# Kernel optimization log

Hardware: AMD Instinct MI355X
Metric: run time of the kernel (lower is better)

Reference implementation:

```python
import jax, jax.numpy as jnp
import numpy as np

PI = jnp.pi
NB_FRAMES = 2


def _axis_angle_to_R(r):
    # r: [..., 3] axis-angle -> rotation matrix [..., 3, 3] (Rodrigues)
    eps = 1e-8
    theta = jnp.sqrt(jnp.sum(r * r, axis=-1, keepdims=True))  # [...,1]
    k = r / jnp.maximum(theta, eps)
    kx, ky, kz = k[..., 0], k[..., 1], k[..., 2]
    zero = jnp.zeros_like(kx)
    K = jnp.stack([
        jnp.stack([zero, -kz, ky], axis=-1),
        jnp.stack([kz, zero, -kx], axis=-1),
        jnp.stack([-ky, kx, zero], axis=-1),
    ], axis=-2)  # [...,3,3]
    I = jnp.eye(3, dtype=r.dtype)
    s = jnp.sin(theta)[..., None]
    c = jnp.cos(theta)[..., None]
    return I + s * K + (1.0 - c) * (K @ K)


def _equirec_dirs(h, w, dtype):
    # unit viewing directions of an equirectangular grid, [h, w, 3]
    lon = ((jnp.arange(w, dtype=dtype) + 0.5) / w * 2.0 - 1.0) * PI
    lat = -((jnp.arange(h, dtype=dtype) + 0.5) / h * 2.0 - 1.0) * (0.5 * PI)
    LON, LAT = jnp.meshgrid(lon, lat)  # [h, w]
    dx = jnp.cos(LAT) * jnp.sin(LON)
    dy = jnp.sin(LAT)
    dz = jnp.cos(LAT) * jnp.cos(LON)
    return jnp.stack([dx, dy, dz], axis=-1)


def _grid_sample(img, grid):
    # img: [B,C,H,W]; grid: [B,Hg,Wg,2] in [-1,1] (x,y); bilinear,
    # align_corners=True, zero padding (matches F.grid_sample defaults)
    B, C, H, W = img.shape
    x = (grid[..., 0] + 1.0) * 0.5 * (W - 1)
    y = (grid[..., 1] + 1.0) * 0.5 * (H - 1)
    x0 = jnp.floor(x)
    y0 = jnp.floor(y)
    x1 = x0 + 1.0
    y1 = y0 + 1.0
    img_flat = img.reshape(B, C, H * W)

    def gather(xi, yi):
        valid = (xi >= 0) & (xi <= W - 1) & (yi >= 0) & (yi <= H - 1)
        xc = jnp.clip(xi, 0, W - 1).astype(jnp.int32)
        yc = jnp.clip(yi, 0, H - 1).astype(jnp.int32)
        idx = (yc * W + xc).reshape(B, 1, -1)
        v = jnp.take_along_axis(img_flat, idx, axis=2).reshape(B, C, *xi.shape[1:])
        return v * valid[:, None].astype(img.dtype)

    wa = ((x1 - x) * (y1 - y))[:, None]
    wb = ((x1 - x) * (y - y0))[:, None]
    wc = ((x - x0) * (y1 - y))[:, None]
    wd = ((x - x0) * (y - y0))[:, None]
    return (gather(x0, y0) * wa + gather(x0, y1) * wb +
            gather(x1, y0) * wc + gather(x1, y1) * wd)


def _area_down(x, s):
    # F.interpolate(mode='area') with integer factor == average pooling
    if s == 1:
        return x
    B, C, H, W = x.shape
    return x.reshape(B, C, H // s, s, W // s, s).mean(axis=(3, 5))


def _photometric_loss(ref_rgb, depths, masks, tgts, pose):
    R = _axis_angle_to_R(pose[..., 3:])      # [B, nb, 3, 3]
    t = pose[..., :3]                         # [B, nb, 3]
    loss = jnp.zeros((), dtype=ref_rgb.dtype)
    for i, (d, m) in enumerate(zip(depths, masks)):
        s = 2 ** i
        h, w = d.shape[2], d.shape[3]
        rr = _area_down(ref_rgb, s)                       # [B,3,h,w]
        tg = [_area_down(tr, s) for tr in tgts]
        dirs = _equirec_dirs(h, w, ref_rgb.dtype)         # [h,w,3]
        xyz = d[:, 0, :, :, None] * dirs[None]            # [B,h,w,3]
        # pose transform: pts = R @ xyz + t  -> [B,h,w,nb,3]
        pts = jnp.einsum('bnij,bhwj->bhwni', R, xyz) + t[:, None, None]
        norm = jnp.sqrt(jnp.sum(pts * pts, axis=-1))
        lon = jnp.arctan2(pts[..., 0], pts[..., 2])
        lat = jnp.arcsin(jnp.clip(pts[..., 1] / jnp.maximum(norm, 1e-8), -1.0, 1.0))
        X = lon / PI                  # [B,h,w,nb]
        Y = lat / (0.5 * PI)
        for j in range(NB_FRAMES):
            coord = jnp.stack([X[..., j], Y[..., j]], axis=-1)  # [B,h,w,2]
            wf = _grid_sample(tg[j], coord)                     # [B,3,h,w]
            loss = loss + jnp.mean(m[:, j:j + 1] * jnp.abs(rr - wf))
    return loss


def setup_inputs() -> dict:
    key = jax.random.key(0)
    ks = jax.random.split(key, 16)
    B, H, W = 8, 512, 1024
    inp = {'ref_rgb': jax.random.uniform(ks[0], (B, 3, H, W), jnp.float32)}
    for i in range(4):
        h, w = H // (2 ** i), W // (2 ** i)
        inp[f'ref_depth{i}'] = jax.random.uniform(ks[1 + i], (B, 1, h, w), jnp.float32)
        inp[f'exp_mask{i}'] = jax.random.uniform(ks[5 + i], (B, NB_FRAMES, h, w), jnp.float32)
    inp['tgt_rgb0'] = jax.random.uniform(ks[9], (B, 3, H, W), jnp.float32)
    inp['tgt_rgb1'] = jax.random.uniform(ks[10], (B, 3, H, W), jnp.float32)
    inp['pose'] = jax.random.normal(ks[11], (B, NB_FRAMES, 6), jnp.float32)
    return inp


def reference(ref_rgb, ref_depth0, ref_depth1, ref_depth2, ref_depth3,
              exp_mask0, exp_mask1, exp_mask2, exp_mask3,
              tgt_rgb0, tgt_rgb1, pose):
    depths = [ref_depth0, ref_depth1, ref_depth2, ref_depth3]
    masks = [exp_mask0, exp_mask1, exp_mask2, exp_mask3]
    tgts = [tgt_rgb0, tgt_rgb1]
    return _photometric_loss(ref_rgb, depths, masks, tgts, pose)
```

## Files before the change

kernel.cpp:

```cpp
#include <hip/hip_runtime.h>
#include <hip/hip_fp16.h>
#include <math.h>

#define PI_F 3.14159265358979323846f

__device__ inline float fast_atan2f(float y, float x) {
    float ax = fabsf(x), ay = fabsf(y);
    float mx = fmaxf(ax, ay);
    float mn = fminf(ax, ay);
    float a = __fdividef(mn, fmaxf(mx, 1e-30f));
    float s = a * a;
    float r = fmaf(s, fmaf(s, fmaf(s, fmaf(s, fmaf(s, -0.01172120f, 0.05265332f),
                   -0.11643287f), 0.19354346f), -0.33262347f), 0.99997726f);
    r = r * a;
    if (ay > ax) r = 1.57079632679f - r;
    if (x < 0.0f) r = PI_F - r;
    return copysignf(r, y);
}

__device__ inline float fast_atanp(float y, float x) {
    float ay = fabsf(y);
    float mx = fmaxf(x, ay);
    float mn = fminf(x, ay);
    float a = __fdividef(mn, fmaxf(mx, 1e-30f));
    float s = a * a;
    float r = fmaf(s, fmaf(s, fmaf(s, fmaf(s, fmaf(s, -0.01172120f, 0.05265332f),
                   -0.11643287f), 0.19354346f), -0.33262347f), 0.99997726f);
    r = r * a;
    if (ay > x) r = 1.57079632679f - r;
    return copysignf(r, y);
}

__device__ inline void make_Rt_to(const float* __restrict__ pose, int bn, float* __restrict__ o) {
    const float* p = pose + bn * 6;
    float tx = p[0], ty = p[1], tz = p[2];
    float rx = p[3], ry = p[4], rz = p[5];
    float theta = sqrtf(rx * rx + ry * ry + rz * rz);
    float inv = __fdividef(1.0f, fmaxf(theta, 1e-8f));
    float kx = rx * inv, ky = ry * inv, kz = rz * inv;
    float s, c;
    __sincosf(theta, &s, &c);
    float oc = 1.0f - c;
    o[0] = 1.0f - oc * (ky * ky + kz * kz);
    o[1] = -s * kz + oc * kx * ky;
    o[2] =  s * ky + oc * kx * kz;
    o[3] =  s * kz + oc * kx * ky;
    o[4] = 1.0f - oc * (kx * kx + kz * kz);
    o[5] = -s * kx + oc * ky * kz;
    o[6] = -s * ky + oc * kx * kz;
    o[7] =  s * kx + oc * ky * kz;
    o[8] = 1.0f - oc * (kx * kx + ky * ky);
    o[9] = tx; o[10] = ty; o[11] = tz;
}

__device__ inline unsigned pack_px1(float r, float g, float b) {
    unsigned ri = __float2uint_rn(__saturatef(r) * 2047.0f);
    unsigned gi = __float2uint_rn(__saturatef(g) * 2047.0f);
    unsigned bi = __float2uint_rn(__saturatef(b) * 1023.0f);
    return ri | (gi << 11) | (bi << 22);
}
__device__ inline float3 unpack_fields(unsigned u) {
    float r = (float)(u & 2047u);
    float g = (float)((u >> 11) & 2047u);
    float b = (float)(u >> 22);
    return make_float3(r, g, b);
}

typedef struct __attribute__((packed, aligned(4))) { unsigned x, y; } upair;

__global__ __launch_bounds__(256) void prep_kernel(
    const float* __restrict__ ref, const float* __restrict__ tgt0, const float* __restrict__ tgt1,
    unsigned* __restrict__ packF,
    unsigned* __restrict__ pL1t, unsigned* __restrict__ pL2t, unsigned* __restrict__ pL3t,
    unsigned* __restrict__ pL1r, unsigned* __restrict__ pL2r, unsigned* __restrict__ pL3r,
    float* __restrict__ out)
{
    int bid = blockIdx.x;
    int t = threadIdx.x;
    if (bid == 0 && t == 0) out[0] = 0.0f;
    int i = bid % 3;
    int rem = bid / 3;
    int b = rem & 7;
    int band = rem >> 3;
    const float* img = (i == 0) ? ref : (i == 1) ? tgt0 : tgt1;
    int x4 = t << 2;
    int y0 = band << 3;
    int q = (i - 1) * 8 + b;

    float l1v[4][2][3];
#pragma unroll
    for (int p = 0; p < 4; ++p) {
        float4 a[3], bb[3];
#pragma unroll
        for (int c = 0; c < 3; ++c) {
            const float* pl = img + ((size_t)(b * 3 + c) << 19);
            a[c]  = *(const float4*)(pl + ((y0 + 2 * p) << 10) + x4);
            bb[c] = *(const float4*)(pl + ((y0 + 2 * p + 1) << 10) + x4);
        }
        if (i > 0) {
            unsigned* o = packF + ((size_t)q << 19) + ((y0 + 2 * p) << 10) + x4;
            uint4 v0;
            v0.x = pack_px1(a[0].x, a[1].x, a[2].x);
            v0.y = pack_px1(a[0].y, a[1].y, a[2].y);
            v0.z = pack_px1(a[0].z, a[1].z, a[2].z);
            v0.w = pack_px1(a[0].w, a[1].w, a[2].w);
            *(uint4*)o = v0;
            unsigned* o2 = o + (1 << 10);
            uint4 v1;
            v1.x = pack_px1(bb[0].x, bb[1].x, bb[2].x);
            v1.y = pack_px1(bb[0].y, bb[1].y, bb[2].y);
            v1.z = pack_px1(bb[0].z, bb[1].z, bb[2].z);
            v1.w = pack_px1(bb[0].w, bb[1].w, bb[2].w);
            *(uint4*)o2 = v1;
        }
#pragma unroll
        for (int c = 0; c < 3; ++c) {
            l1v[p][0][c] = (a[c].x + a[c].y + bb[c].x + bb[c].y) * 0.25f;
            l1v[p][1][c] = (a[c].z + a[c].w + bb[c].z + bb[c].w) * 0.25f;
        }
        uint2 d;
        d.x = pack_px1(l1v[p][0][0], l1v[p][0][1], l1v[p][0][2]);
        d.y = pack_px1(l1v[p][1][0], l1v[p][1][1], l1v[p][1][2]);
        unsigned* d1 = ((i == 0) ? pL1r + ((size_t)b << 17) : pL1t + ((size_t)q << 17))
                    + (((band << 2) + p) << 9) + (t << 1);
        *(uint2*)d1 = d;
    }
    float l2v[2][3];
#pragma unroll
    for (int pr = 0; pr < 2; ++pr) {
#pragma unroll
        for (int c = 0; c < 3; ++c)
            l2v[pr][c] = (l1v[2 * pr][0][c] + l1v[2 * pr][1][c] +
                          l1v[2 * pr + 1][0][c] + l1v[2 * pr + 1][1][c]) * 0.25f;
        unsigned* d2 = ((i == 0) ? pL2r + ((size_t)b << 15) : pL2t + ((size_t)q << 15))
                    + (((band << 1) + pr) << 8) + t;
        *d2 = pack_px1(l2v[pr][0], l2v[pr][1], l2v[pr][2]);
    }
    float l3[3];
#pragma unroll
    for (int c = 0; c < 3; ++c) {
        float s = l2v[0][c] + l2v[1][c];
        l3[c] = (s + __shfl_xor(s, 1)) * 0.25f;
    }
    if ((t & 1) == 0) {
        unsigned* d3 = ((i == 0) ? pL3r + ((size_t)b << 13) : pL3t + ((size_t)q << 13))
                    + (band << 7) + (t >> 1);
        *d3 = pack_px1(l3[0], l3[1], l3[2]);
    }
}

template <int SH>
__device__ inline float photo_scale4(int bidl, int tid,
                                     const float* __restrict__ rrF,
                                     const unsigned* __restrict__ rrP,
                                     const float* __restrict__ depth,
                                     const float* __restrict__ mask,
                                     const unsigned* __restrict__ tg,
                                     const float* __restrict__ pose,
                                     float* __restrict__ ldsRt) {
    constexpr int h = 512 >> SH;
    constexpr int w = 1024 >> SH;
    constexpr int LOG2W = 10 - SH;
    constexpr int LP = 19 - 2 * SH;
    constexpr float inv_count = 1.0f / (8.0f * 3.0f * h * w);
    constexpr float GXS = (float)((w - 1) / (2.0 * 3.14159265358979323846));
    constexpr float GXB = (float)((w - 1) * 0.5);
    constexpr float GYS = (float)((h - 1) / 3.14159265358979323846);
    constexpr float GYB = (float)((h - 1) * 0.5);
    constexpr float CDs[4] = {0.9999811752826011f, 0.9999247018391445f,
                              0.9996988186962042f, 0.9987954562051724f};
    constexpr float SDs[4] = {0.006135884649154475f, 0.012271538285719925f,
                              0.024541228522912288f, 0.049067674327418015f};
    constexpr float CD = CDs[SH], SD = SDs[SH];

    int lidx = ((bidl << 8) + tid) << 2;
    int b = lidx >> LP;
    if (tid < 2) make_Rt_to(pose, b * 2 + tid, ldsRt + tid * 12);
    __syncthreads();

    int x0 = lidx & (w - 1);
    int y = (lidx >> LOG2W) & (h - 1);
    int pix = (y << LOG2W) + x0;

    float lat = -(((float)y + 0.5f) * (2.0f / (float)h) - 1.0f) * (0.5f * PI_F);
    float slat = __sinf(lat), clat = __cosf(lat);

    float4 dep4 = *(const float4*)(depth + ((size_t)b << LP) + pix);
    float dp[4] = {dep4.x, dep4.y, dep4.z, dep4.w};
    float rcv[4][3];
    if constexpr (SH == 0) {
#pragma unroll
        for (int c = 0; c < 3; ++c) {
            float F = (c == 2) ? 1023.0f : 2047.0f;
            float4 rv = *(const float4*)(rrF + ((size_t)(b * 3 + c) << LP) + pix);
            rcv[0][c] = rv.x * F; rcv[1][c] = rv.y * F;
            rcv[2][c] = rv.z * F; rcv[3][c] = rv.w * F;
        }
    } else {
        const unsigned* rp = rrP + ((size_t)b << LP) + pix;
        uint4 u = *(const uint4*)rp;
        float3 f0 = unpack_fields(u.x), f1 = unpack_fields(u.y);
        float3 f2 = unpack_fields(u.z), f3 = unpack_fields(u.w);
        rcv[0][0] = f0.x; rcv[0][1] = f0.y; rcv[0][2] = f0.z;
        rcv[1][0] = f1.x; rcv[1][1] = f1.y; rcv[1][2] = f1.z;
        rcv[2][0] = f2.x; rcv[2][1] = f2.y; rcv[2][2] = f2.z;
        rcv[3][0] = f3.x; rcv[3][1] = f3.y; rcv[3][2] = f3.z;
    }
    float m4[2][4];
#pragma unroll
    for (int n = 0; n < 2; ++n) {
        float4 mv = *(const float4*)(mask + ((size_t)(b * 2 + n) << LP) + pix);
        m4[n][0] = mv.x; m4[n][1] = mv.y; m4[n][2] = mv.z; m4[n][3] = mv.w;
    }

    const unsigned* pl0 = tg + ((size_t)b << LP);
    const unsigned* pl1 = tg + ((size_t)(8 + b) << LP);

    float fxv[8], fyv[8];
    int off2[8][2];
    float lon0 = (((float)x0 + 0.5f) * (2.0f / (float)w) - 1.0f) * PI_F;
    float sl, cl;
    __sincosf(lon0, &sl, &cl);
#pragma unroll
    for (int i = 0; i < 4; ++i) {
        if (i > 0) {
            float s2 = fmaf(sl, CD, cl * SD);
            float c2 = fmaf(cl, CD, -sl * SD);
            sl = s2; cl = c2;
        }
        float X = dp[i] * (clat * sl);
        float Y = dp[i] * slat;
        float Z = dp[i] * (clat * cl);
#pragma unroll
        for (int n = 0; n < 2; ++n) {
            const float* R = ldsRt + n * 12;
            float px = fmaf(R[0], X, fmaf(R[1], Y, fmaf(R[2], Z, R[9])));
            float py = fmaf(R[3], X, fmaf(R[4], Y, fmaf(R[5], Z, R[10])));
            float pz = fmaf(R[6], X, fmaf(R[7], Y, fmaf(R[8], Z, R[11])));
            float rxz2 = fmaf(px, px, pz * pz);
            float rxz = rxz2 * __frsqrt_rn(fmaxf(rxz2, 1e-30f));
            float lon2 = fast_atan2f(px, pz);
            float lat2 = fast_atanp(py, rxz);
            float gx = fmaf(lon2, GXS, GXB);
            float gy = fmaf(lat2, GYS, GYB);
            float x0f = floorf(gx), y0f = floorf(gy);
            int xi0 = max((int)x0f, 0);
            int yi0 = max((int)y0f, 0);
            int yi1 = min(yi0 + 1, h - 1);
            int g = i * 2 + n;
            fxv[g] = gx - x0f;
            fyv[g] = gy - y0f;
            off2[g][0] = (yi0 << LOG2W) + xi0;
            off2[g][1] = (yi1 << LOG2W) + xi0;
        }
    }
    upair tp[8][2];
#pragma unroll
    for (int g = 0; g < 8; ++g) {
        const unsigned* P = (g & 1) ? pl1 : pl0;
        tp[g][0] = *(const upair*)(P + off2[g][0]);
        tp[g][1] = *(const upair*)(P + off2[g][1]);
    }
    float acc = 0.0f;
#pragma unroll
    for (int g = 0; g < 8; ++g) {
        int i = g >> 1, n = g & 1;
        float fx = fxv[g], fy = fyv[g];
        float ofx = 1.0f - fx, ofy = 1.0f - fy;
        float w00 = ofx * ofy;
        float w01 = ofx * fy;
        float w10 = fx * ofy;
        float w11 = fx * fy;
        float3 ta = unpack_fields(tp[g][0].x);
        float3 tc = unpack_fields(tp[g][0].y);
        float3 tb = unpack_fields(tp[g][1].x);
        float3 td = unpack_fields(tp[g][1].y);
        float d0 = rcv[i][0] - (fmaf(w00, ta.x, fmaf(w01, tb.x, fmaf(w10, tc.x, w11 * td.x))));
        float d1 = rcv[i][1] - (fmaf(w00, ta.y, fmaf(w01, tb.y, fmaf(w10, tc.y, w11 * td.y))));
        float d2 = rcv[i][2] - (fmaf(w00, ta.z, fmaf(w01, tb.z, fmaf(w10, tc.z, w11 * td.z))));
        float t = fabsf(d0) * (1.0f / 2047.0f);
        t = fmaf(fabsf(d1), (1.0f / 2047.0f), t);
        t = fmaf(fabsf(d2), (1.0f / 1023.0f), t);
        acc = fmaf(m4[n][i], t, acc);
    }
    return acc * inv_count;
}

__global__ __launch_bounds__(256) void photo_all_packed4q(
    const float* __restrict__ rrF,
    const unsigned* __restrict__ rr1, const unsigned* __restrict__ rr2, const unsigned* __restrict__ rr3,
    const float* __restrict__ dep0, const float* __restrict__ msk0,
    const float* __restrict__ dep1, const float* __restrict__ msk1,
    const float* __restrict__ dep2, const float* __restrict__ msk2,
    const float* __restrict__ dep3, const float* __restrict__ msk3,
    const unsigned* __restrict__ packF,
    const unsigned* __restrict__ pL1t, const unsigned* __restrict__ pL2t, const unsigned* __restrict__ pL3t,
    const float* __restrict__ pose, float* __restrict__ out) {
    __shared__ float ldsRt[24];
    __shared__ float wsum[4];
    int bid = blockIdx.x, tid = threadIdx.x;
    float acc;
    if (bid < 4096) {
        int s = ((bid & 7) << 9) | (bid >> 3);
        acc = photo_scale4<0>(s, tid, rrF, nullptr, dep0, msk0, packF, pose, ldsRt);
    } else if (bid < 5120) {
        int t0 = bid - 4096;
        int s = ((t0 & 7) << 7) | (t0 >> 3);
        acc = photo_scale4<1>(s, tid, nullptr, rr1, dep1, msk1, pL1t, pose, ldsRt);
    } else if (bid < 5376) {
        int t0 = bid - 5120;
        int s = ((t0 & 7) << 5) | (t0 >> 3);
        acc = photo_scale4<2>(s, tid, nullptr, rr2, dep2, msk2, pL2t, pose, ldsRt);
    } else {
        int t0 = bid - 5376;
        int s = ((t0 & 7) << 3) | (t0 >> 3);
        acc = photo_scale4<3>(s, tid, nullptr, rr3, dep3, msk3, pL3t, pose, ldsRt);
    }

    for (int off = 32; off > 0; off >>= 1) acc += __shfl_down(acc, off);
    if ((tid & 63) == 0) wsum[tid >> 6] = acc;
    __syncthreads();
    if (tid == 0) atomicAdd(out, wsum[0] + wsum[1] + wsum[2] + wsum[3]);
}

template <int LWD>
__global__ __launch_bounds__(256) void down3_kernel(const float* __restrict__ sA,
                                                    const float* __restrict__ sB,
                                                    const float* __restrict__ sC,
                                                    float* __restrict__ dA,
                                                    float* __restrict__ dB,
                                                    float* __restrict__ dC) {
    const float* src = (blockIdx.y == 0) ? sA : (blockIdx.y == 1) ? sB : sC;
    float* dst = (blockIdx.y == 0) ? dA : (blockIdx.y == 1) ? dB : dC;
    int idx = blockIdx.x * 256 + threadIdx.x;
    constexpr int HB = LWD - 1;
    int xp = idx & ((1 << HB) - 1);
    int y = (idx >> HB) & ((1 << HB) - 1);
    int c = idx >> (2 * HB);
    const float* sp = src + ((size_t)c << (2 * LWD + 1)) + ((size_t)(2 * y) << (LWD + 1)) + 4 * xp;
    float4 r0 = *(const float4*)sp;
    float4 r1 = *(const float4*)(sp + (1 << (LWD + 1)));
    float2 d;
    d.x = 0.25f * (r0.x + r0.y + r1.x + r1.y);
    d.y = 0.25f * (r0.z + r0.w + r1.z + r1.w);
    *(float2*)(dst + ((size_t)c << (2 * LWD - 1)) + ((size_t)y << LWD) + 2 * xp) = d;
}

template <int SH>
__device__ inline float photo_scale(int bidl, int tid,
                                    const float* __restrict__ rr,
                                    const float* __restrict__ depth,
                                    const float* __restrict__ mask,
                                    const float* __restrict__ tg0,
                                    const float* __restrict__ tg1,
                                    const float* __restrict__ pose,
                                    float* __restrict__ ldsRt) {
    constexpr int h = 512 >> SH;
    constexpr int w = 1024 >> SH;
    constexpr int LOG2W = 10 - SH;
    constexpr int LP = 19 - 2 * SH;
    constexpr float inv_count = 1.0f / (8.0f * 3.0f * h * w);
    int lidx = (bidl << 8) + tid;
    int b = lidx >> LP;
    if (tid < 2) make_Rt_to(pose, b * 2 + tid, ldsRt + tid * 12);
    __syncthreads();
    int x = lidx & (w - 1);
    int y = (lidx >> LOG2W) & (h - 1);
    int pix = (y << LOG2W) + x;
    float lon = (((float)x + 0.5f) * (2.0f / (float)w) - 1.0f) * PI_F;
    float lat = -(((float)y + 0.5f) * (2.0f / (float)h) - 1.0f) * (0.5f * PI_F);
    float sl = __sinf(lon), cl = __cosf(lon);
    float slat = __sinf(lat), clat = __cosf(lat);
    float dep = depth[((size_t)b << LP) + pix];
    float X = dep * clat * sl, Y = dep * slat, Z = dep * clat * cl;
    float rc[3];
#pragma unroll
    for (int c = 0; c < 3; ++c)
        rc[c] = rr[((size_t)(b * 3 + c) << LP) + pix];
    float acc = 0.0f;
#pragma unroll
    for (int n = 0; n < 2; ++n) {
        const float* R = ldsRt + n * 12;
        float px = R[0] * X + R[1] * Y + R[2] * Z + R[9];
        float py = R[3] * X + R[4] * Y + R[5] * Z + R[10];
        float pz = R[6] * X + R[7] * Y + R[8] * Z + R[11];
        float rxz = sqrtf(px * px + pz * pz);
        float lon2 = fast_atan2f(px, pz);
        float lat2 = fast_atan2f(py, rxz);
        float gx = (lon2 * (1.0f / PI_F) + 1.0f) * 0.5f * (float)(w - 1);
        float gy = (lat2 * (2.0f / PI_F) + 1.0f) * 0.5f * (float)(h - 1);
        float x0f = floorf(gx), y0f = floorf(gy);
        float fx = gx - x0f, fy = gy - y0f;
        float wa = (1.0f - fx) * (1.0f - fy);
        float wb = (1.0f - fx) * fy;
        float wc = fx * (1.0f - fy);
        float wd = fx * fy;
        bool vx0 = (x0f >= 0.0f) && (x0f <= (float)(w - 1));
        bool vx1 = (x0f >= -1.0f) && (x0f <= (float)(w - 2));
        bool vy0 = (y0f >= 0.0f) && (y0f <= (float)(h - 1));
        bool vy1 = (y0f >= -1.0f) && (y0f <= (float)(h - 2));
        int xi0 = (int)fminf(fmaxf(x0f, 0.0f), (float)(w - 1));
        int xi1 = (int)fminf(fmaxf(x0f + 1.0f, 0.0f), (float)(w - 1));
        int yi0 = (int)fminf(fmaxf(y0f, 0.0f), (float)(h - 1));
        int yi1 = (int)fminf(fmaxf(y0f + 1.0f, 0.0f), (float)(h - 1));
        float waf = (vx0 && vy0) ? wa : 0.0f;
        float wbf = (vx0 && vy1) ? wb : 0.0f;
        float wcf = (vx1 && vy0) ? wc : 0.0f;
        float wdf = (vx1 && vy1) ? wd : 0.0f;
        int ia = (yi0 << LOG2W) + xi0;
        int ib2 = (yi1 << LOG2W) + xi0;
        int ic = (yi0 << LOG2W) + xi1;
        int id = (yi1 << LOG2W) + xi1;
        const float* tg = (n == 0) ? tg0 : tg1;
        float m = mask[((size_t)(b * 2 + n) << LP) + pix];
#pragma unroll
        for (int c = 0; c < 3; ++c) {
            const float* plane = tg + ((size_t)(b * 3 + c) << LP);
            float v = waf * plane[ia] + wbf * plane[ib2] + wcf * plane[ic] + wdf * plane[id];
            acc += m * fabsf(rc[c] - v);
        }
    }
    return acc * inv_count;
}

__global__ __launch_bounds__(256) void photo_all_kernel(
    const float* __restrict__ rr0, const float* __restrict__ dep0, const float* __restrict__ msk0,
    const float* __restrict__ tA0, const float* __restrict__ tB0,
    const float* __restrict__ rr1, const float* __restrict__ dep1, const float* __restrict__ msk1,
    const float* __restrict__ tA1, const float* __restrict__ tB1,
    const float* __restrict__ rr2, const float* __restrict__ dep2, const float* __restrict__ msk2,
    const float* __restrict__ tA2, const float* __restrict__ tB2,
    const float* __restrict__ rr3, const float* __restrict__ dep3, const float* __restrict__ msk3,
    const float* __restrict__ tA3, const float* __restrict__ tB3,
    const float* __restrict__ pose, float* __restrict__ out) {
    __shared__ float ldsRt[24];
    __shared__ float wsum[4];
    int bid = blockIdx.x, tid = threadIdx.x;
    float acc;
    if (bid < 16384)
        acc = photo_scale<0>(bid, tid, rr0, dep0, msk0, tA0, tB0, pose, ldsRt);
    else if (bid < 20480)
        acc = photo_scale<1>(bid - 16384, tid, rr1, dep1, msk1, tA1, tB1, pose, ldsRt);
    else if (bid < 21504)
        acc = photo_scale<2>(bid - 20480, tid, rr2, dep2, msk2, tA2, tB2, pose, ldsRt);
    else
        acc = photo_scale<3>(bid - 21504, tid, rr3, dep3, msk3, tA3, tB3, pose, ldsRt);
    for (int off = 32; off > 0; off >>= 1) acc += __shfl_down(acc, off);
    if ((tid & 63) == 0) wsum[tid >> 6] = acc;
    __syncthreads();
    if (tid == 0) atomicAdd(out, wsum[0] + wsum[1] + wsum[2] + wsum[3]);
}

extern "C" void kernel_launch(void* const* d_in, const int* in_sizes, int n_in,
                              void* d_out, int out_size, void* d_ws, size_t ws_size,
                              hipStream_t stream) {
    const float* ref  = (const float*)d_in[0];
    const float* dep0 = (const float*)d_in[1];
    const float* msk0 = (const float*)d_in[2];
    const float* dep1 = (const float*)d_in[3];
    const float* msk1 = (const float*)d_in[4];
    const float* dep2 = (const float*)d_in[5];
    const float* msk2 = (const float*)d_in[6];
    const float* dep3 = (const float*)d_in[7];
    const float* msk3 = (const float*)d_in[8];
    const float* tgt0 = (const float*)d_in[9];
    const float* tgt1 = (const float*)d_in[10];
    const float* pose = (const float*)d_in[11];
    float* out = (float*)d_out;

    const size_t E_F   = (size_t)16 << 19;
    const size_t E_L1t = (size_t)16 << 17;
    const size_t E_L2t = (size_t)16 << 15;
    const size_t E_L3t = (size_t)16 << 13;
    const size_t E_L1r = (size_t)8 << 17;
    const size_t E_L2r = (size_t)8 << 15;
    const size_t E_L3r = (size_t)8 << 13;
    const size_t NEED_PACKED = (E_F + E_L1t + E_L2t + E_L3t + E_L1r + E_L2r + E_L3r) * sizeof(unsigned);

    const size_t L1 = (size_t)24 * 256 * 512;
    const size_t L2 = (size_t)24 * 128 * 256;
    const size_t L3 = (size_t)24 * 64 * 128;
    const size_t NEED_A = 3 * (L1 + L2 + L3) * sizeof(float);

    if (ws_size >= NEED_PACKED) {
        unsigned* p = (unsigned*)d_ws;
        unsigned* packF = p; p += E_F;
        unsigned* pL1t = p; p += E_L1t;
        unsigned* pL2t = p; p += E_L2t;
        unsigned* pL3t = p; p += E_L3t;
        unsigned* pL1r = p; p += E_L1r;
        unsigned* pL2r = p; p += E_L2r;
        unsigned* pL3r = p; p += E_L3r;

        prep_kernel<<<1536, 256, 0, stream>>>(ref, tgt0, tgt1, packF,
                                              pL1t, pL2t, pL3t, pL1r, pL2r, pL3r, out);
        photo_all_packed4q<<<5440, 256, 0, stream>>>(
            ref, pL1r, pL2r, pL3r,
            dep0, msk0, dep1, msk1, dep2, msk2, dep3, msk3,
            packF, pL1t, pL2t, pL3t, pose, out);
    } else if (ws_size >= NEED_A) {
        hipMemsetAsync(out, 0, sizeof(float), stream);
        float* p = (float*)d_ws;
        float* ref_l1 = p; p += L1;
        float* ref_l2 = p; p += L2;
        float* ref_l3 = p; p += L3;
        float* t0_l1 = p; p += L1;
        float* t0_l2 = p; p += L2;
        float* t0_l3 = p; p += L3;
        float* t1_l1 = p; p += L1;
        float* t1_l2 = p; p += L2;
        float* t1_l3 = p; p += L3;
        down3_kernel<9><<<dim3((24 << 16) / 256, 3), 256, 0, stream>>>(
            ref, tgt0, tgt1, ref_l1, t0_l1, t1_l1);
        down3_kernel<8><<<dim3((24 << 14) / 256, 3), 256, 0, stream>>>(
            ref_l1, t0_l1, t1_l1, ref_l2, t0_l2, t1_l2);
        down3_kernel<7><<<dim3((24 << 12) / 256, 3), 256, 0, stream>>>(
            ref_l2, t0_l2, t1_l2, ref_l3, t0_l3, t1_l3);
        photo_all_kernel<<<21760, 256, 0, stream>>>(
            ref, dep0, msk0, tgt0, tgt1,
            ref_l1, dep1, msk1, t0_l1, t1_l1,
            ref_l2, dep2, msk2, t0_l2, t1_l2,
            ref_l3, dep3, msk3, t0_l3, t1_l3,
            pose, out);
    }
}
```

Measured before the change: 306.0 us.

## Interleave row pairs in packed target pyramids for single 16-byte bilinear fetches

The prep kernel now stores packed target images with row pairs interleaved, so each 16-byte chunk holds a 2x2 pixel block (rows 2k and 2k+1, two adjacent columns). The photometric kernel fetches a 16-byte quad per bilinear row and picks the needed elements by row parity. The goal is fewer, wider and more cache-friendly gathers for the bilinear taps. In exchange it issues wider loads that can be misaligned when the x index is odd, and adds select logic. The prep writes for every pyramid level change to the new layout.

```diff
diff --git a/kernel.cpp b/kernel.cpp
--- a/kernel.cpp
+++ b/kernel.cpp
@@ -66,7 +66,7 @@
     return make_float3(r, g, b);
 }
 
-typedef struct __attribute__((packed, aligned(4))) { unsigned x, y; } upair;
+typedef struct __attribute__((packed, aligned(8))) { unsigned x, y, z, w; } uquad;
 
 __global__ __launch_bounds__(256) void prep_kernel(
     const float* __restrict__ ref, const float* __restrict__ tgt0, const float* __restrict__ tgt1,
@@ -88,6 +88,7 @@
     int q = (i - 1) * 8 + b;
 
     float l1v[4][2][3];
+    unsigned pk1[4][2];
 #pragma unroll
     for (int p = 0; p < 4; ++p) {
         float4 a[3], bb[3];
@@ -98,43 +99,57 @@
             bb[c] = *(const float4*)(pl + ((y0 + 2 * p + 1) << 10) + x4);
         }
         if (i > 0) {
-            unsigned* o = packF + ((size_t)q << 19) + ((y0 + 2 * p) << 10) + x4;
-            uint4 v0;
+            unsigned* o = packF + ((size_t)q << 19)
+                          + ((size_t)(((band << 2) + p)) << 11) + (x4 << 1);
+            uint4 v0, v1;
             v0.x = pack_px1(a[0].x, a[1].x, a[2].x);
-            v0.y = pack_px1(a[0].y, a[1].y, a[2].y);
-            v0.z = pack_px1(a[0].z, a[1].z, a[2].z);
-            v0.w = pack_px1(a[0].w, a[1].w, a[2].w);
+            v0.y = pack_px1(bb[0].x, bb[1].x, bb[2].x);
+            v0.z = pack_px1(a[0].y, a[1].y, a[2].y);
+            v0.w = pack_px1(bb[0].y, bb[1].y, bb[2].y);
+            v1.x = pack_px1(a[0].z, a[1].z, a[2].z);
+            v1.y = pack_px1(bb[0].z, bb[1].z, bb[2].z);
+            v1.z = pack_px1(a[0].w, a[1].w, a[2].w);
+            v1.w = pack_px1(bb[0].w, bb[1].w, bb[2].w);
             *(uint4*)o = v0;
-            unsigned* o2 = o + (1 << 10);
-            uint4 v1;
-            v1.x = pack_px1(bb[0].x, bb[1].x, bb[2].x);
-            v1.y = pack_px1(bb[0].y, bb[1].y, bb[2].y);
-            v1.z = pack_px1(bb[0].z, bb[1].z, bb[2].z);
-            v1.w = pack_px1(bb[0].w, bb[1].w, bb[2].w);
-            *(uint4*)o2 = v1;
+            *(uint4*)(o + 4) = v1;
         }
 #pragma unroll
         for (int c = 0; c < 3; ++c) {
             l1v[p][0][c] = (a[c].x + a[c].y + bb[c].x + bb[c].y) * 0.25f;
             l1v[p][1][c] = (a[c].z + a[c].w + bb[c].z + bb[c].w) * 0.25f;
         }
-        uint2 d;
-        d.x = pack_px1(l1v[p][0][0], l1v[p][0][1], l1v[p][0][2]);
-        d.y = pack_px1(l1v[p][1][0], l1v[p][1][1], l1v[p][1][2]);
-        unsigned* d1 = ((i == 0) ? pL1r + ((size_t)b << 17) : pL1t + ((size_t)q << 17))
-                    + (((band << 2) + p) << 9) + (t << 1);
-        *(uint2*)d1 = d;
+        pk1[p][0] = pack_px1(l1v[p][0][0], l1v[p][0][1], l1v[p][0][2]);
+        pk1[p][1] = pack_px1(l1v[p][1][0], l1v[p][1][1], l1v[p][1][2]);
+        if (i == 0) {
+            uint2 d; d.x = pk1[p][0]; d.y = pk1[p][1];
+            *(uint2*)(pL1r + ((size_t)b << 17) + (((band << 2) + p) << 9) + (t << 1)) = d;
+        }
+    }
+    if (i > 0) {
+#pragma unroll
+        for (int pp = 0; pp < 2; ++pp) {
+            uint4 v;
+            v.x = pk1[2 * pp][0];     v.y = pk1[2 * pp + 1][0];
+            v.z = pk1[2 * pp][1];     v.w = pk1[2 * pp + 1][1];
+            *(uint4*)(pL1t + ((size_t)q << 17) + (((band << 1) + pp) << 10) + (t << 2)) = v;
+        }
     }
     float l2v[2][3];
+    unsigned pk2[2];
 #pragma unroll
     for (int pr = 0; pr < 2; ++pr) {
 #pragma unroll
         for (int c = 0; c < 3; ++c)
             l2v[pr][c] = (l1v[2 * pr][0][c] + l1v[2 * pr][1][c] +
                           l1v[2 * pr + 1][0][c] + l1v[2 * pr + 1][1][c]) * 0.25f;
-        unsigned* d2 = ((i == 0) ? pL2r + ((size_t)b << 15) : pL2t + ((size_t)q << 15))
-                    + (((band << 1) + pr) << 8) + t;
-        *d2 = pack_px1(l2v[pr][0], l2v[pr][1], l2v[pr][2]);
+        pk2[pr] = pack_px1(l2v[pr][0], l2v[pr][1], l2v[pr][2]);
+        if (i == 0) {
+            pL2r[((size_t)b << 15) + (((band << 1) + pr) << 8) + t] = pk2[pr];
+        }
+    }
+    if (i > 0) {
+        uint2 d; d.x = pk2[0]; d.y = pk2[1];
+        *(uint2*)(pL2t + ((size_t)q << 15) + (band << 9) + (t << 1)) = d;
     }
     float l3[3];
 #pragma unroll
@@ -143,9 +158,12 @@
         l3[c] = (s + __shfl_xor(s, 1)) * 0.25f;
     }
     if ((t & 1) == 0) {
-        unsigned* d3 = ((i == 0) ? pL3r + ((size_t)b << 13) : pL3t + ((size_t)q << 13))
-                    + (band << 7) + (t >> 1);
-        *d3 = pack_px1(l3[0], l3[1], l3[2]);
+        unsigned v = pack_px1(l3[0], l3[1], l3[2]);
+        if (i == 0) {
+            pL3r[((size_t)b << 13) + (band << 7) + (t >> 1)] = v;
+        } else {
+            pL3t[((size_t)q << 13) + ((band >> 1) << 8) + t + (band & 1)] = v;
+        }
     }
 }
 
@@ -217,7 +235,8 @@
     const unsigned* pl1 = tg + ((size_t)(8 + b) << LP);
 
     float fxv[8], fyv[8];
-    int off2[8][2];
+    int offq[8][2];
+    int prv[8];
     float lon0 = (((float)x0 + 0.5f) * (2.0f / (float)w) - 1.0f) * PI_F;
     float sl, cl;
     __sincosf(lon0, &sl, &cl);
@@ -250,43 +269,50 @@
             int g = i * 2 + n;
             fxv[g] = gx - x0f;
             fyv[g] = gy - y0f;
-            off2[g][0] = (yi0 << LOG2W) + xi0;
-            off2[g][1] = (yi1 << LOG2W) + xi0;
-        }
-    }
-    upair tp[8][2];
+            offq[g][0] = ((yi0 >> 1) << (LOG2W + 1)) + (xi0 << 1);
+            offq[g][1] = ((yi1 >> 1) << (LOG2W + 1)) + (xi0 << 1);
+            prv[g] = (yi0 & 1) | ((yi1 & 1) << 1);
+        }
+    }
+    uquad tq[8][2];
 #pragma unroll
     for (int g = 0; g < 8; ++g) {
         const unsigned* P = (g & 1) ? pl1 : pl0;
-        tp[g][0] = *(const upair*)(P + off2[g][0]);
-        tp[g][1] = *(const upair*)(P + off2[g][1]);
+        tq[g][0] = *(const uquad*)(P + offq[g][0]);
+        tq[g][1] = *(const uquad*)(P + offq[g][1]);
     }
     float acc = 0.0f;
 #pragma unroll
     for (int g = 0; g < 8; ++g) {
         int i = g >> 1, n = g & 1;
+        bool par0 = (prv[g] & 1) != 0;
+        bool par1 = (prv[g] & 2) != 0;
+        unsigned e_ta = par0 ? tq[g][0].y : tq[g][0].x;
+        unsigned e_tc = par0 ? tq[g][0].w : tq[g][0].z;
+        unsigned e_tb = par1 ? tq[g][1].y : tq[g][1].x;
+        unsigned e_td = par1 ? tq[g][1].w : tq[g][1].z;
         float fx = fxv[g], fy = fyv[g];
         float ofx = 1.0f - fx, ofy = 1.0f - fy;
         float w00 = ofx * ofy;
         float w01 = ofx * fy;
         float w10 = fx * ofy;
         float w11 = fx * fy;
-        float3 ta = unpack_fields(tp[g][0].x);
-        float3 tc = unpack_fields(tp[g][0].y);
-        float3 tb = unpack_fields(tp[g][1].x);
-        float3 td = unpack_fields(tp[g][1].y);
+        float3 ta = unpack_fields(e_ta);
+        float3 tb = unpack_fields(e_tb);
+        float3 tc = unpack_fields(e_tc);
+        float3 td = unpack_fields(e_td);
         float d0 = rcv[i][0] - (fmaf(w00, ta.x, fmaf(w01, tb.x, fmaf(w10, tc.x, w11 * td.x))));
         float d1 = rcv[i][1] - (fmaf(w00, ta.y, fmaf(w01, tb.y, fmaf(w10, tc.y, w11 * td.y))));
         float d2 = rcv[i][2] - (fmaf(w00, ta.z, fmaf(w01, tb.z, fmaf(w10, tc.z, w11 * td.z))));
-        float t = fabsf(d0) * (1.0f / 2047.0f);
-        t = fmaf(fabsf(d1), (1.0f / 2047.0f), t);
-        t = fmaf(fabsf(d2), (1.0f / 1023.0f), t);
-        acc = fmaf(m4[n][i], t, acc);
+        float tsum = fabsf(d0) * (1.0f / 2047.0f);
+        tsum = fmaf(fabsf(d1), (1.0f / 2047.0f), tsum);
+        tsum = fmaf(fabsf(d2), (1.0f / 1023.0f), tsum);
+        acc = fmaf(m4[n][i], tsum, acc);
     }
     return acc * inv_count;
 }
 
-__global__ __launch_bounds__(256) void photo_all_packed4q(
+__global__ __launch_bounds__(256) void photo_all_packed4s(
     const float* __restrict__ rrF,
     const unsigned* __restrict__ rr1, const unsigned* __restrict__ rr2, const unsigned* __restrict__ rr3,
     const float* __restrict__ dep0, const float* __restrict__ msk0,
@@ -494,7 +520,7 @@
 
         prep_kernel<<<1536, 256, 0, stream>>>(ref, tgt0, tgt1, packF,
                                               pL1t, pL2t, pL3t, pL1r, pL2r, pL3r, out);
-        photo_all_packed4q<<<5440, 256, 0, stream>>>(
+        photo_all_packed4s<<<5440, 256, 0, stream>>>(
             ref, pL1r, pL2r, pL3r,
             dep0, msk0, dep1, msk1, dep2, msk2, dep3, msk3,
             packF, pL1t, pL2t, pL3t, pose, out);
```

Result: slower. 406.5 us (+32.8%).
